# Optimization experiments

Hardware: AMD Instinct MI355X
Metric: run time of the kernel (lower is better)

Reference implementation:

```python
import jax, jax.numpy as jnp
import numpy as np

B, LMAX, T_OUT, VOCAB, EMB, CVEC, HID, OUT = 8192, 12, 10, 36, 300, 256, 256, 512


def setup_inputs() -> dict:
    key = jax.random.key(0)
    ks = jax.random.split(key, 16)
    s = lambda fan: 1.0 / np.sqrt(fan)
    u = lambda k, shape, b: jax.random.uniform(k, shape, jnp.float32, -b, b)
    inp = {
        'words': jax.random.randint(ks[0], (B, LMAX), 0, VOCAB),
        'lengths': 1 + jax.random.randint(ks[1], (B,), 0, LMAX),  # in [1, LMAX]
        'emb_table': jax.random.normal(ks[2], (VOCAB, EMB), jnp.float32),
        'enc_w': u(ks[3], (CVEC, EMB), s(EMB)),
        'enc_b': u(ks[4], (CVEC,), s(EMB)),
        'wih_f': u(ks[5], (4 * HID, CVEC), s(HID)),
        'whh_f': u(ks[6], (4 * HID, HID), s(HID)),
        'bih_f': u(ks[7], (4 * HID,), s(HID)),
        'bhh_f': u(ks[8], (4 * HID,), s(HID)),
        'wih_b': u(ks[9], (4 * HID, CVEC), s(HID)),
        'whh_b': u(ks[10], (4 * HID, HID), s(HID)),
        'bih_b': u(ks[11], (4 * HID,), s(HID)),
        'bhh_b': u(ks[12], (4 * HID,), s(HID)),
        'out_w': u(ks[13], (OUT, 2 * HID), s(2 * HID)),
        'out_b': u(ks[14], (OUT,), s(2 * HID)),
    }
    return inp


def _interp_words(emb_table, words, lengths):
    # bilinear resize (L,300)->(10,300) with align_corners=True; width unchanged
    # so it is exact linear interpolation along the char axis.
    def one(word_row, L):
        Lf = (L - 1).astype(jnp.float32)
        pos = jnp.arange(T_OUT, dtype=jnp.float32) * Lf / (T_OUT - 1)  # (10,)
        i0 = jnp.floor(pos).astype(jnp.int32)
        i1 = jnp.minimum(i0 + 1, L - 1).astype(jnp.int32)
        f = (pos - i0.astype(jnp.float32))[:, None]
        e = emb_table[word_row]  # (LMAX, EMB)
        return e[i0] * (1.0 - f) + e[i1] * f  # (10, EMB)
    return jax.vmap(one)(words, lengths)  # (B, 10, EMB)


def _lstm(seq, wih, whh, bih, bhh):
    # seq: (T, B, In); PyTorch gate order i, f, g, o
    bsz = seq.shape[1]
    h0 = jnp.zeros((bsz, HID), seq.dtype)
    c0 = jnp.zeros((bsz, HID), seq.dtype)

    def step(carry, x_t):
        h, c = carry
        g = x_t @ wih.T + h @ whh.T + (bih + bhh)
        i, f, gg, o = jnp.split(g, 4, axis=-1)
        c = jax.nn.sigmoid(f) * c + jax.nn.sigmoid(i) * jnp.tanh(gg)
        h = jax.nn.sigmoid(o) * jnp.tanh(c)
        return (h, c), h

    _, hs = jax.lax.scan(step, (h0, c0), seq)
    return hs  # (T, B, HID)


def reference(words, lengths, emb_table, enc_w, enc_b, wih_f, whh_f, bih_f, bhh_f,
              wih_b, whh_b, bih_b, bhh_b, out_w, out_b):
    emb = _interp_words(emb_table, words, lengths)              # (B, 10, 300)
    cv = jax.nn.relu(emb @ enc_w.T + enc_b)                     # (B, 10, 256)
    seq = jnp.transpose(cv, (1, 0, 2))                          # (10, B, 256)
    h_f = _lstm(seq, wih_f, whh_f, bih_f, bhh_f)                # (10, B, 256)
    h_b = _lstm(seq[::-1], wih_b, whh_b, bih_b, bhh_b)[::-1]    # (10, B, 256)
    rec = jnp.concatenate([h_f, h_b], axis=-1)                  # (10, B, 512)
    out = rec @ out_w.T + out_b                                 # (10, B, 512)
    return jnp.transpose(out, (1, 0, 2))                        # (B, 10, 512)
```

## Files before the change

### kernel.cpp

```cpp
#include <hip/hip_runtime.h>
#include <hip/hip_fp16.h>

typedef _Float16 f16;
typedef _Float16 f16x2 __attribute__((ext_vector_type(2)));
typedef _Float16 f16x8 __attribute__((ext_vector_type(8)));
typedef float    f32x4 __attribute__((ext_vector_type(4)));

#define NB   8192
#define TOUT 10
#define LMAX 12
#define EMB  300

__device__ __forceinline__ float sigm_(float x) {
    return __builtin_amdgcn_rcpf(1.0f + __builtin_amdgcn_exp2f(x * -1.44269504f));
}
__device__ __forceinline__ float tanh_(float x) {
    return 1.0f - 2.0f * __builtin_amdgcn_rcpf(1.0f + __builtin_amdgcn_exp2f(x * 2.88539008f));
}
__device__ __forceinline__ f16x2 pk_f16(float a, float b) {
    return __builtin_bit_cast(f16x2, __builtin_amdgcn_cvt_pkrtz(a, b));
}

__device__ __forceinline__ void gl_lds16(const f16* g, f16* l) {
    __builtin_amdgcn_global_load_lds(
        (const __attribute__((address_space(1))) void*)g,
        (__attribute__((address_space(3))) void*)l, 16, 0, 0);
}

__global__ __launch_bounds__(256) void pack_w2(
    const float* __restrict__ wih_f, const float* __restrict__ whh_f,
    const float* __restrict__ wih_b, const float* __restrict__ whh_b,
    f16* __restrict__ Wp) {
    int idx = blockIdx.x * 256 + threadIdx.x;
    int d   = idx >> 19;
    int r   = idx & 524287;
    int tile = r >> 9;
    int e    = r & 511;
    int kc = tile >> 6, nt = tile & 63;
    int khi = e >> 7, rem = e & 127, nl = rem >> 3, klo = rem & 7;
    int n = nt * 16 + nl;
    int k = kc * 32 + khi * 8 + klo;
    int gate = (n >> 4) & 3;
    int u = ((n >> 6) << 4) | (n & 15);
    int srow = gate * 256 + u;
    const float* wih = d ? wih_b : wih_f;
    const float* whh = d ? whh_b : whh_f;
    float v = (k < 256) ? wih[srow * 256 + k] : whh[srow * 256 + (k - 256)];
    Wp[idx] = (f16)v;
}

__global__ __launch_bounds__(256) void pack_bias(
    const float* __restrict__ bih_f, const float* __restrict__ bhh_f,
    const float* __restrict__ bih_b, const float* __restrict__ bhh_b,
    float* __restrict__ bp) {
    int idx = blockIdx.x * 256 + threadIdx.x;
    int d = idx >> 10, n = idx & 1023;
    int gate = (n >> 4) & 3;
    int u = ((n >> 6) << 4) | (n & 15);
    int srow = gate * 256 + u;
    bp[idx] = d ? (bih_b[srow] + bhh_b[srow]) : (bih_f[srow] + bhh_f[srow]);
}

__global__ __launch_bounds__(256) void pack_w3(
    const float* __restrict__ out_w, f16* __restrict__ W3p) {
    int idx = blockIdx.x * 256 + threadIdx.x;
    int tile = idx >> 9, e = idx & 511;
    int kc = tile >> 5, nt = tile & 31;
    int khi = e >> 7, rem = e & 127, nl = rem >> 3, klo = rem & 7;
    int n = nt * 16 + nl, k = kc * 32 + khi * 8 + klo;
    W3p[idx] = (f16)out_w[n * 512 + k];
}

__global__ __launch_bounds__(256) void enc_proj(
    const float* __restrict__ tab, const float* __restrict__ ew,
    const float* __restrict__ eb, float* __restrict__ P) {
    int v = blockIdx.x, j = threadIdx.x;
    const float* a = tab + v * EMB;
    const float* w = ew + j * EMB;
    float s = 0.0f;
    for (int k = 0; k < EMB; ++k) s += a[k] * w[k];
    P[v * 256 + j] = s + eb[j];
}

__global__ __launch_bounds__(256) void build_seq(
    const int* __restrict__ words, const int* __restrict__ lengths,
    const float* __restrict__ P, f16* __restrict__ seqp) {
    int gi = blockIdx.x * 256 + threadIdx.x;
    int bl  = gi & 15;
    int khi = (gi >> 4) & 3;
    int kc  = (gi >> 6) & 7;
    int mt  = (gi >> 9) & 511;
    int t   = gi >> 18;
    int b = mt * 16 + bl;
    int L = lengths[b];
    float pos = ((float)t * (float)(L - 1)) / 9.0f;
    int i0 = (int)pos;
    float f = pos - (float)i0;
    int i1 = min(i0 + 1, L - 1);
    int c0 = words[b * LMAX + i0];
    int c1 = words[b * LMAX + i1];
    const float* p0 = P + c0 * 256 + kc * 32 + khi * 8;
    const float* p1 = P + c1 * 256 + kc * 32 + khi * 8;
    f16x8 r;
#pragma unroll
    for (int j = 0; j < 8; ++j) {
        float v = p0[j] * (1.0f - f) + p1[j] * f;
        v = fmaxf(v, 0.0f);
        r[j] = (f16)v;
    }
    *((f16x8*)seqp + gi) = r;
}

__global__ __launch_bounds__(1024) void lstm_fused(
    const f16* __restrict__ seqp, const f16* __restrict__ Wp,
    const float* __restrict__ bp, f16* __restrict__ hcat) {
    const int dir  = blockIdx.x >> 7;
    const int r0t  = (blockIdx.x & 127) << 2;
    const int wave = threadIdx.x >> 6;
    const int lane = threadIdx.x & 63;
    const int l16  = lane & 15;
    const int quad = lane >> 4;

    __shared__ __align__(16) f16 hbuf[2][16384];
    __shared__ __align__(16) f16 sbuf[2][16384];

    {
        f16x8 z = {(f16)0, (f16)0, (f16)0, (f16)0, (f16)0, (f16)0, (f16)0, (f16)0};
        for (int i = threadIdx.x; i < 2048; i += 1024) ((f16x8*)hbuf[0])[i] = z;
    }

    {
        const int t0 = dir ? 9 : 0;
        const f16* s0 = seqp + (size_t)(t0 * 512 + r0t) * 4096;
        gl_lds16(s0 + threadIdx.x * 8,        &sbuf[0][wave * 512]);
        gl_lds16(s0 + 8192 + threadIdx.x * 8, &sbuf[0][8192 + wave * 512]);
    }

    const float* bpd = bp + dir * 1024 + wave * 64;
    float bias_l[4];
#pragma unroll
    for (int nt = 0; nt < 4; ++nt) bias_l[nt] = bpd[nt * 16 + l16];

    const f16* Wu = Wp + dir * 524288 + wave * 2048;
    const int  wo = lane * 8;

    const int slot = wave >> 1;
    const int ofs0 = (((wave & 1) * 2 + (l16 >> 3)) * 16 + quad * 4) * 8 + (l16 & 7);
    const int tile_lo = (r0t * 16 + dir * 8 + slot) * 512;

    float cst[4][4];
#pragma unroll
    for (int m = 0; m < 4; ++m)
#pragma unroll
        for (int q = 0; q < 4; ++q) cst[m][q] = 0.0f;

    __syncthreads();

    int cur = 0;
#pragma unroll 1
    for (int step = 0; step < TOUT; ++step) {
        const int t = dir ? (9 - step) : step;

        if (step != 9) {
            const int tn = dir ? (t - 1) : (t + 1);
            const f16* ns = seqp + (size_t)(tn * 512 + r0t) * 4096;
            gl_lds16(ns + threadIdx.x * 8,        &sbuf[cur ^ 1][wave * 512]);
            gl_lds16(ns + 8192 + threadIdx.x * 8, &sbuf[cur ^ 1][8192 + wave * 512]);
        }

        const f16* sb   = &sbuf[cur][lane * 8];
        const f16* hb_r = &hbuf[cur][lane * 8];
        f16*       hb_w = hbuf[cur ^ 1];

        f32x4 acc[4][4];
#pragma unroll
        for (int m = 0; m < 4; ++m)
#pragma unroll
            for (int nt = 0; nt < 4; ++nt)
#pragma unroll
                for (int q = 0; q < 4; ++q) acc[m][nt][q] = bias_l[nt];

#pragma unroll 1
        for (int kc = 0; kc < 8; ++kc) {
            const f16* wk = Wu + kc * 32768;
            f16x8 bfrag[4];
#pragma unroll
            for (int nt = 0; nt < 4; ++nt)
                bfrag[nt] = *(const f16x8*)(wk + nt * 512 + wo);
            f16x8 afrag[4];
#pragma unroll
            for (int m = 0; m < 4; ++m)
                afrag[m] = *(const f16x8*)(sb + (m * 8 + kc) * 512);
            __builtin_amdgcn_s_setprio(1);
#pragma unroll
            for (int m = 0; m < 4; ++m)
#pragma unroll
                for (int nt = 0; nt < 4; ++nt)
                    acc[m][nt] = __builtin_amdgcn_mfma_f32_16x16x32_f16(
                        afrag[m], bfrag[nt], acc[m][nt], 0, 0, 0);
            __builtin_amdgcn_s_setprio(0);
        }
#pragma unroll 1
        for (int kcl = 0; kcl < 8; ++kcl) {
            const f16* wk = Wu + (kcl + 8) * 32768;
            f16x8 bfrag[4];
#pragma unroll
            for (int nt = 0; nt < 4; ++nt)
                bfrag[nt] = *(const f16x8*)(wk + nt * 512 + wo);
            f16x8 afrag[4];
#pragma unroll
            for (int m = 0; m < 4; ++m)
                afrag[m] = *(const f16x8*)(hb_r + (m * 8 + kcl) * 512);
            __builtin_amdgcn_s_setprio(1);
#pragma unroll
            for (int m = 0; m < 4; ++m)
#pragma unroll
                for (int nt = 0; nt < 4; ++nt)
                    acc[m][nt] = __builtin_amdgcn_mfma_f32_16x16x32_f16(
                        afrag[m], bfrag[nt], acc[m][nt], 0, 0, 0);
            __builtin_amdgcn_s_setprio(0);
        }

        f16* hct = hcat + ((size_t)t * 4194304 + tile_lo);
#pragma unroll
        for (int m = 0; m < 4; ++m) {
#pragma unroll
            for (int q = 0; q < 4; ++q) {
                float iv = acc[m][0][q];
                float fv = acc[m][1][q];
                float gv = acc[m][2][q];
                float ov = acc[m][3][q];
                float c = sigm_(fv) * cst[m][q] + sigm_(iv) * tanh_(gv);
                cst[m][q] = c;
                f16 hv = (f16)(sigm_(ov) * tanh_(c));
                int wt = ofs0 + q * 8;
                hb_w[(m * 8 + slot) * 512 + wt] = hv;
                hct[m * 8192 + wt] = hv;
            }
        }

        __syncthreads();
        cur ^= 1;
    }
}

__global__ __launch_bounds__(512) void out_gemm(
    const f16* __restrict__ hcat, const f16* __restrict__ W3p,
    const float* __restrict__ out_b, float* __restrict__ out) {
    const int mt0  = blockIdx.x << 2;
    const int wave = threadIdx.x >> 6;
    const int lane = threadIdx.x & 63;
    const int l16  = lane & 15;
    const int quad = lane >> 4;
    const int n0   = wave * 64;

    float bias_l[4];
#pragma unroll
    for (int nt = 0; nt < 4; ++nt) bias_l[nt] = out_b[n0 + nt * 16 + l16];

    f32x4 acc[4][4];
#pragma unroll
    for (int m = 0; m < 4; ++m)
#pragma unroll
        for (int nt = 0; nt < 4; ++nt)
#pragma unroll
            for (int q = 0; q < 4; ++q) acc[m][nt][q] = bias_l[nt];

#pragma unroll 2
    for (int kc = 0; kc < 16; ++kc) {
        f16x8 a[4], b[4];
#pragma unroll
        for (int m = 0; m < 4; ++m)
            a[m] = *(const f16x8*)(hcat + ((size_t)((mt0 + m) * 16 + kc) * 512 + lane * 8));
#pragma unroll
        for (int nt = 0; nt < 4; ++nt)
            b[nt] = *(const f16x8*)(W3p + ((kc * 32 + wave * 4 + nt) * 512 + lane * 8));
#pragma unroll
        for (int m = 0; m < 4; ++m)
#pragma unroll
            for (int nt = 0; nt < 4; ++nt)
                acc[m][nt] = __builtin_amdgcn_mfma_f32_16x16x32_f16(a[m], b[nt], acc[m][nt], 0, 0, 0);
    }

#pragma unroll
    for (int m = 0; m < 4; ++m) {
#pragma unroll
        for (int nt = 0; nt < 4; ++nt) {
#pragma unroll
            for (int q = 0; q < 4; ++q) {
                int R = mt0 * 16 + m * 16 + quad * 4 + q;
                int t = R >> 13;
                int b = R & 8191;
                out[(size_t)(b * 10 + t) * 512 + n0 + nt * 16 + l16] = acc[m][nt][q];
            }
        }
    }
}

extern "C" void kernel_launch(void* const* d_in, const int* in_sizes, int n_in,
                              void* d_out, int out_size, void* d_ws, size_t ws_size,
                              hipStream_t stream) {
    const int*   words   = (const int*)d_in[0];
    const int*   lengths = (const int*)d_in[1];
    const float* tab     = (const float*)d_in[2];
    const float* enc_w   = (const float*)d_in[3];
    const float* enc_b   = (const float*)d_in[4];
    const float* wih_f   = (const float*)d_in[5];
    const float* whh_f   = (const float*)d_in[6];
    const float* bih_f   = (const float*)d_in[7];
    const float* bhh_f   = (const float*)d_in[8];
    const float* wih_b   = (const float*)d_in[9];
    const float* whh_b   = (const float*)d_in[10];
    const float* bih_b   = (const float*)d_in[11];
    const float* bhh_b   = (const float*)d_in[12];
    const float* out_w   = (const float*)d_in[13];
    const float* out_b   = (const float*)d_in[14];
    float* out = (float*)d_out;

    char* ws = (char*)d_ws;
    f16*   Wp   = (f16*)(ws + 0);
    f16*   W3p  = (f16*)(ws + 2097152);
    float* bp   = (float*)(ws + 2621440);
    float* P    = (float*)(ws + 2629632);
    f16*   seqp = (f16*)(ws + 2666496);
    f16*   hcat = (f16*)(ws + 44609536);

    pack_w2<<<4096, 256, 0, stream>>>(wih_f, whh_f, wih_b, whh_b, Wp);
    pack_bias<<<8, 256, 0, stream>>>(bih_f, bhh_f, bih_b, bhh_b, bp);
    pack_w3<<<1024, 256, 0, stream>>>(out_w, W3p);
    enc_proj<<<36, 256, 0, stream>>>(tab, enc_w, enc_b, P);
    build_seq<<<10240, 256, 0, stream>>>(words, lengths, P, seqp);
    lstm_fused<<<256, 1024, 0, stream>>>(seqp, Wp, bp, hcat);
    out_gemm<<<1280, 512, 0, stream>>>(hcat, W3p, out_b, out);
}
```

Baseline: 456.4 us.

## Stream LSTM weight fragments through LDS ring with async global-to-LDS loads

Weight B-fragments are no longer loaded straight from global into registers. Each wave now streams them through a small three-slot LDS ring using global_load_lds, with explicit vmcnt waits so the next fragment's load overlaps the current MFMAs. The k-loop is restructured to do the recurrent h part first, then the input sequence part. The sequence tile becomes single-buffered and is loaded at the start of each step instead of prefetched during the previous one. This trades register pressure and global load latency for more LDS traffic and fine-grained waits, and it risks exposing the sequence-load latency and the LDS slot reuse ordering.

```diff
diff --git a/kernel.cpp b/kernel.cpp
--- a/kernel.cpp
+++ b/kernel.cpp
@@ -17,15 +17,14 @@
 __device__ __forceinline__ float tanh_(float x) {
     return 1.0f - 2.0f * __builtin_amdgcn_rcpf(1.0f + __builtin_amdgcn_exp2f(x * 2.88539008f));
 }
-__device__ __forceinline__ f16x2 pk_f16(float a, float b) {
-    return __builtin_bit_cast(f16x2, __builtin_amdgcn_cvt_pkrtz(a, b));
-}
 
 __device__ __forceinline__ void gl_lds16(const f16* g, f16* l) {
     __builtin_amdgcn_global_load_lds(
         (const __attribute__((address_space(1))) void*)g,
         (__attribute__((address_space(3))) void*)l, 16, 0, 0);
 }
+
+#define WAITV(n) asm volatile("s_waitcnt vmcnt(" #n ")" ::: "memory")
 
 __global__ __launch_bounds__(256) void pack_w2(
     const float* __restrict__ wih_f, const float* __restrict__ whh_f,
@@ -122,27 +121,22 @@
     const int quad = lane >> 4;
 
     __shared__ __align__(16) f16 hbuf[2][16384];
-    __shared__ __align__(16) f16 sbuf[2][16384];
+    __shared__ __align__(16) f16 sbuf[16384];
+    __shared__ __align__(16) f16 wbuf[24576];
 
     {
         f16x8 z = {(f16)0, (f16)0, (f16)0, (f16)0, (f16)0, (f16)0, (f16)0, (f16)0};
         for (int i = threadIdx.x; i < 2048; i += 1024) ((f16x8*)hbuf[0])[i] = z;
     }
 
-    {
-        const int t0 = dir ? 9 : 0;
-        const f16* s0 = seqp + (size_t)(t0 * 512 + r0t) * 4096;
-        gl_lds16(s0 + threadIdx.x * 8,        &sbuf[0][wave * 512]);
-        gl_lds16(s0 + 8192 + threadIdx.x * 8, &sbuf[0][8192 + wave * 512]);
-    }
-
     const float* bpd = bp + dir * 1024 + wave * 64;
     float bias_l[4];
 #pragma unroll
     for (int nt = 0; nt < 4; ++nt) bias_l[nt] = bpd[nt * 16 + l16];
 
-    const f16* Wu = Wp + dir * 524288 + wave * 2048;
-    const int  wo = lane * 8;
+    const f16* wsrc = Wp + dir * 524288 + wave * 2048 + lane * 8;
+    f16*       wdst = wbuf + wave * 1536;
+    const f16* wred = wdst + lane * 8;
 
     const int slot = wave >> 1;
     const int ofs0 = (((wave & 1) * 2 + (l16 >> 3)) * 16 + quad * 4) * 8 + (l16 & 7);
@@ -161,17 +155,19 @@
     for (int step = 0; step < TOUT; ++step) {
         const int t = dir ? (9 - step) : step;
 
-        if (step != 9) {
-            const int tn = dir ? (t - 1) : (t + 1);
-            const f16* ns = seqp + (size_t)(tn * 512 + r0t) * 4096;
-            gl_lds16(ns + threadIdx.x * 8,        &sbuf[cur ^ 1][wave * 512]);
-            gl_lds16(ns + 8192 + threadIdx.x * 8, &sbuf[cur ^ 1][8192 + wave * 512]);
-        }
-
-        const f16* sb   = &sbuf[cur][lane * 8];
+        const f16* sb   = &sbuf[lane * 8];
         const f16* hb_r = &hbuf[cur][lane * 8];
         f16*       hb_w = hbuf[cur ^ 1];
 
+        {
+            const f16* ss = seqp + (size_t)(t * 512 + r0t) * 4096;
+            gl_lds16(ss + threadIdx.x * 8,        &sbuf[wave * 512]);
+            gl_lds16(ss + 8192 + threadIdx.x * 8, &sbuf[8192 + wave * 512]);
+        }
+        gl_lds16(wsrc + 8 * 32768 + 0 * 512, wdst + 0 * 512);
+        gl_lds16(wsrc + 8 * 32768 + 1 * 512, wdst + 1 * 512);
+        gl_lds16(wsrc + 8 * 32768 + 2 * 512, wdst + 2 * 512);
+
         f32x4 acc[4][4];
 #pragma unroll
         for (int m = 0; m < 4; ++m)
@@ -180,45 +176,109 @@
 #pragma unroll
                 for (int q = 0; q < 4; ++q) acc[m][nt][q] = bias_l[nt];
 
+        int jm = 0;
 #pragma unroll 1
-        for (int kc = 0; kc < 8; ++kc) {
-            const f16* wk = Wu + kc * 32768;
-            f16x8 bfrag[4];
-#pragma unroll
-            for (int nt = 0; nt < 4; ++nt)
-                bfrag[nt] = *(const f16x8*)(wk + nt * 512 + wo);
+        for (int j = 0; j < 15; ++j) {
+            const f16* ab = (j < 8) ? hb_r : (sb - 4096);
             f16x8 afrag[4];
 #pragma unroll
             for (int m = 0; m < 4; ++m)
-                afrag[m] = *(const f16x8*)(sb + (m * 8 + kc) * 512);
-            __builtin_amdgcn_s_setprio(1);
+                afrag[m] = *(const f16x8*)(ab + (m * 8 + j) * 512);
+
+            int s0 = jm;
+            int s1 = jm + 1; if (s1 >= 3) s1 -= 3;
+            int s2 = jm + 2; if (s2 >= 3) s2 -= 3;
+            const f16* wn0 = wsrc + ((j      ^ 8) * 32768);
+            const f16* wn1 = wsrc + (((j + 1) ^ 8) * 32768);
+
+            WAITV(2);
+            {
+                f16x8 b = *(const f16x8*)(wred + s0 * 512);
+                __builtin_amdgcn_s_setprio(1);
+#pragma unroll
+                for (int m = 0; m < 4; ++m)
+                    acc[m][0] = __builtin_amdgcn_mfma_f32_16x16x32_f16(afrag[m], b, acc[m][0], 0, 0, 0);
+                __builtin_amdgcn_s_setprio(0);
+                gl_lds16(wn0 + 3 * 512, wdst + s0 * 512);
+            }
+            WAITV(2);
+            {
+                f16x8 b = *(const f16x8*)(wred + s1 * 512);
+                __builtin_amdgcn_s_setprio(1);
+#pragma unroll
+                for (int m = 0; m < 4; ++m)
+                    acc[m][1] = __builtin_amdgcn_mfma_f32_16x16x32_f16(afrag[m], b, acc[m][1], 0, 0, 0);
+                __builtin_amdgcn_s_setprio(0);
+                gl_lds16(wn1 + 0 * 512, wdst + s1 * 512);
+            }
+            WAITV(2);
+            {
+                f16x8 b = *(const f16x8*)(wred + s2 * 512);
+                __builtin_amdgcn_s_setprio(1);
+#pragma unroll
+                for (int m = 0; m < 4; ++m)
+                    acc[m][2] = __builtin_amdgcn_mfma_f32_16x16x32_f16(afrag[m], b, acc[m][2], 0, 0, 0);
+                __builtin_amdgcn_s_setprio(0);
+                gl_lds16(wn1 + 1 * 512, wdst + s2 * 512);
+            }
+            WAITV(2);
+            {
+                f16x8 b = *(const f16x8*)(wred + s0 * 512);
+                __builtin_amdgcn_s_setprio(1);
+#pragma unroll
+                for (int m = 0; m < 4; ++m)
+                    acc[m][3] = __builtin_amdgcn_mfma_f32_16x16x32_f16(afrag[m], b, acc[m][3], 0, 0, 0);
+                __builtin_amdgcn_s_setprio(0);
+                gl_lds16(wn1 + 2 * 512, wdst + s0 * 512);
+            }
+            jm = (jm == 2) ? 0 : jm + 1;
+        }
+
+        {
+            const f16* ab = sb - 4096;
+            f16x8 afrag[4];
 #pragma unroll
             for (int m = 0; m < 4; ++m)
-#pragma unroll
-                for (int nt = 0; nt < 4; ++nt)
-                    acc[m][nt] = __builtin_amdgcn_mfma_f32_16x16x32_f16(
-                        afrag[m], bfrag[nt], acc[m][nt], 0, 0, 0);
-            __builtin_amdgcn_s_setprio(0);
-        }
-#pragma unroll 1
-        for (int kcl = 0; kcl < 8; ++kcl) {
-            const f16* wk = Wu + (kcl + 8) * 32768;
-            f16x8 bfrag[4];
-#pragma unroll
-            for (int nt = 0; nt < 4; ++nt)
-                bfrag[nt] = *(const f16x8*)(wk + nt * 512 + wo);
-            f16x8 afrag[4];
-#pragma unroll
-            for (int m = 0; m < 4; ++m)
-                afrag[m] = *(const f16x8*)(hb_r + (m * 8 + kcl) * 512);
-            __builtin_amdgcn_s_setprio(1);
-#pragma unroll
-            for (int m = 0; m < 4; ++m)
-#pragma unroll
-                for (int nt = 0; nt < 4; ++nt)
-                    acc[m][nt] = __builtin_amdgcn_mfma_f32_16x16x32_f16(
-                        afrag[m], bfrag[nt], acc[m][nt], 0, 0, 0);
-            __builtin_amdgcn_s_setprio(0);
+                afrag[m] = *(const f16x8*)(ab + (m * 8 + 15) * 512);
+            const f16* wn0 = wsrc + 7 * 32768;
+
+            WAITV(2);
+            {
+                f16x8 b = *(const f16x8*)(wred + 0 * 512);
+                __builtin_amdgcn_s_setprio(1);
+#pragma unroll
+                for (int m = 0; m < 4; ++m)
+                    acc[m][0] = __builtin_amdgcn_mfma_f32_16x16x32_f16(afrag[m], b, acc[m][0], 0, 0, 0);
+                __builtin_amdgcn_s_setprio(0);
+                gl_lds16(wn0 + 3 * 512, wdst + 0 * 512);
+            }
+            WAITV(2);
+            {
+                f16x8 b = *(const f16x8*)(wred + 1 * 512);
+                __builtin_amdgcn_s_setprio(1);
+#pragma unroll
+                for (int m = 0; m < 4; ++m)
+                    acc[m][1] = __builtin_amdgcn_mfma_f32_16x16x32_f16(afrag[m], b, acc[m][1], 0, 0, 0);
+                __builtin_amdgcn_s_setprio(0);
+            }
+            WAITV(1);
+            {
+                f16x8 b = *(const f16x8*)(wred + 2 * 512);
+                __builtin_amdgcn_s_setprio(1);
+#pragma unroll
+                for (int m = 0; m < 4; ++m)
+                    acc[m][2] = __builtin_amdgcn_mfma_f32_16x16x32_f16(afrag[m], b, acc[m][2], 0, 0, 0);
+                __builtin_amdgcn_s_setprio(0);
+            }
+            WAITV(0);
+            {
+                f16x8 b = *(const f16x8*)(wred + 0 * 512);
+                __builtin_amdgcn_s_setprio(1);
+#pragma unroll
+                for (int m = 0; m < 4; ++m)
+                    acc[m][3] = __builtin_amdgcn_mfma_f32_16x16x32_f16(afrag[m], b, acc[m][3], 0, 0, 0);
+                __builtin_amdgcn_s_setprio(0);
+            }
         }
 
         f16* hct = hcat + ((size_t)t * 4194304 + tile_lo);
```

Measured after the change: 551.3 us. +20.8%, slower.

## Stream LSTM weights through double-buffered LDS and coalesce hidden-state stores

Applied to the files above, without the earlier changes.

The LSTM kernel previously read weight fragments directly from global memory inside each k-chunk loop. It now stages them into a double-buffered LDS area with async global_load_lds, explicitly pipelined over 32 unrolled phases with vmcnt waits. The h and sequence buffers become single-buffered, separated by explicit barriers. The scattered per-element hcat stores are replaced by coalesced 16-byte copies of the previous step's h from LDS. This aims to hide weight-load latency and cut uncoalesced writes, at the cost of more barriers per step and tighter ordering of the vmcnt counts.

```diff
diff --git a/kernel.cpp b/kernel.cpp
--- a/kernel.cpp
+++ b/kernel.cpp
@@ -17,15 +17,14 @@
 __device__ __forceinline__ float tanh_(float x) {
     return 1.0f - 2.0f * __builtin_amdgcn_rcpf(1.0f + __builtin_amdgcn_exp2f(x * 2.88539008f));
 }
-__device__ __forceinline__ f16x2 pk_f16(float a, float b) {
-    return __builtin_bit_cast(f16x2, __builtin_amdgcn_cvt_pkrtz(a, b));
-}
 
 __device__ __forceinline__ void gl_lds16(const f16* g, f16* l) {
     __builtin_amdgcn_global_load_lds(
         (const __attribute__((address_space(1))) void*)g,
         (__attribute__((address_space(3))) void*)l, 16, 0, 0);
 }
+
+#define WAITV(n) asm volatile("s_waitcnt vmcnt(" #n ")" ::: "memory")
 
 __global__ __launch_bounds__(256) void pack_w2(
     const float* __restrict__ wih_f, const float* __restrict__ whh_f,
@@ -121,19 +120,19 @@
     const int l16  = lane & 15;
     const int quad = lane >> 4;
 
-    __shared__ __align__(16) f16 hbuf[2][16384];
-    __shared__ __align__(16) f16 sbuf[2][16384];
+    __shared__ __align__(16) f16 hbuf[16384];
+    __shared__ __align__(16) f16 sbuf[16384];
+    __shared__ __align__(16) f16 wbuf[2][16384];
 
     {
         f16x8 z = {(f16)0, (f16)0, (f16)0, (f16)0, (f16)0, (f16)0, (f16)0, (f16)0};
-        for (int i = threadIdx.x; i < 2048; i += 1024) ((f16x8*)hbuf[0])[i] = z;
-    }
-
+        for (int i = threadIdx.x; i < 2048; i += 1024) ((f16x8*)hbuf)[i] = z;
+    }
     {
         const int t0 = dir ? 9 : 0;
         const f16* s0 = seqp + (size_t)(t0 * 512 + r0t) * 4096;
-        gl_lds16(s0 + threadIdx.x * 8,        &sbuf[0][wave * 512]);
-        gl_lds16(s0 + 8192 + threadIdx.x * 8, &sbuf[0][8192 + wave * 512]);
+        gl_lds16(s0 + threadIdx.x * 8,        &sbuf[wave * 512]);
+        gl_lds16(s0 + 8192 + threadIdx.x * 8, &sbuf[8192 + wave * 512]);
     }
 
     const float* bpd = bp + dir * 1024 + wave * 64;
@@ -141,12 +140,15 @@
 #pragma unroll
     for (int nt = 0; nt < 4; ++nt) bias_l[nt] = bpd[nt * 16 + l16];
 
-    const f16* Wu = Wp + dir * 524288 + wave * 2048;
-    const int  wo = lane * 8;
+    const f16* Wsl = Wp + dir * 524288 + wave * 2048 + lane * 8;
+    f16*       wds = &wbuf[0][wave * 1024];
+    const f16* wbr = &wbuf[0][wave * 1024 + lane * 8];
+
+    const f16* sbl = sbuf + lane * 8;
+    const f16* hbl = hbuf + lane * 8;
 
     const int slot = wave >> 1;
     const int ofs0 = (((wave & 1) * 2 + (l16 >> 3)) * 16 + quad * 4) * 8 + (l16 & 7);
-    const int tile_lo = (r0t * 16 + dir * 8 + slot) * 512;
 
     float cst[4][4];
 #pragma unroll
@@ -154,74 +156,94 @@
 #pragma unroll
         for (int q = 0; q < 4; ++q) cst[m][q] = 0.0f;
 
+    gl_lds16(Wsl + 0 * 512, wds);
+    gl_lds16(Wsl + 1 * 512, wds + 512);
+    gl_lds16(Wsl + 2 * 512, wds + 16384);
+    gl_lds16(Wsl + 3 * 512, wds + 16384 + 512);
+
     __syncthreads();
 
-    int cur = 0;
+#define PHASE(P)  do {                                                         \
+    if ((P) == 31) { WAITV(0); } else { WAITV(2); }                            \
+    const f16* br_ = wbr + ((P) & 1) * 16384;                                  \
+    f16x8 b0_ = *(const f16x8*)(br_);                                          \
+    f16x8 b1_ = *(const f16x8*)(br_ + 512);                                    \
+    if (((P) & 1) == 0) {                                                      \
+        const f16* ab_ = (((P) >> 1) < 8) ? sbl : hbl;                         \
+        const int ko_ = ((P) >> 1) & 7;                                        \
+        af0 = *(const f16x8*)(ab_ + (0 * 8 + ko_) * 512);                      \
+        af1 = *(const f16x8*)(ab_ + (1 * 8 + ko_) * 512);                      \
+        af2 = *(const f16x8*)(ab_ + (2 * 8 + ko_) * 512);                      \
+        af3 = *(const f16x8*)(ab_ + (3 * 8 + ko_) * 512);                      \
+    }                                                                          \
+    __builtin_amdgcn_s_setprio(1);                                             \
+    acc[0][((P)&1)*2]   = __builtin_amdgcn_mfma_f32_16x16x32_f16(af0, b0_, acc[0][((P)&1)*2],   0,0,0); \
+    acc[1][((P)&1)*2]   = __builtin_amdgcn_mfma_f32_16x16x32_f16(af1, b0_, acc[1][((P)&1)*2],   0,0,0); \
+    acc[2][((P)&1)*2]   = __builtin_amdgcn_mfma_f32_16x16x32_f16(af2, b0_, acc[2][((P)&1)*2],   0,0,0); \
+    acc[3][((P)&1)*2]   = __builtin_amdgcn_mfma_f32_16x16x32_f16(af3, b0_, acc[3][((P)&1)*2],   0,0,0); \
+    acc[0][((P)&1)*2+1] = __builtin_amdgcn_mfma_f32_16x16x32_f16(af0, b1_, acc[0][((P)&1)*2+1], 0,0,0); \
+    acc[1][((P)&1)*2+1] = __builtin_amdgcn_mfma_f32_16x16x32_f16(af1, b1_, acc[1][((P)&1)*2+1], 0,0,0); \
+    acc[2][((P)&1)*2+1] = __builtin_amdgcn_mfma_f32_16x16x32_f16(af2, b1_, acc[2][((P)&1)*2+1], 0,0,0); \
+    acc[3][((P)&1)*2+1] = __builtin_amdgcn_mfma_f32_16x16x32_f16(af3, b1_, acc[3][((P)&1)*2+1], 0,0,0); \
+    __builtin_amdgcn_s_setprio(0);                                             \
+    if ((P) < 30) {                                                            \
+        f16* wd_ = wds + ((P) & 1) * 16384;                                    \
+        gl_lds16(Wsl + ((((P) + 2) >> 1) * 64 + (((P) + 2) & 1) * 2) * 512,       wd_);       \
+        gl_lds16(Wsl + ((((P) + 2) >> 1) * 64 + (((P) + 2) & 1) * 2 + 1) * 512,   wd_ + 512); \
+    }                                                                          \
+} while (0)
+
+    int step = 0;
 #pragma unroll 1
-    for (int step = 0; step < TOUT; ++step) {
+    for (; step < TOUT; ++step) {
         const int t = dir ? (9 - step) : step;
 
+        f32x4 acc[4][4];
+#pragma unroll
+        for (int m = 0; m < 4; ++m)
+#pragma unroll
+            for (int nt = 0; nt < 4; ++nt)
+#pragma unroll
+                for (int q = 0; q < 4; ++q) acc[m][nt][q] = bias_l[nt];
+
+        f16x8 af0, af1, af2, af3;
+
+        PHASE(0);  PHASE(1);  PHASE(2);  PHASE(3);
+        PHASE(4);  PHASE(5);  PHASE(6);  PHASE(7);
+        PHASE(8);  PHASE(9);  PHASE(10); PHASE(11);
+        PHASE(12); PHASE(13); PHASE(14); PHASE(15);
+
+        __builtin_amdgcn_s_barrier();
         if (step != 9) {
             const int tn = dir ? (t - 1) : (t + 1);
             const f16* ns = seqp + (size_t)(tn * 512 + r0t) * 4096;
-            gl_lds16(ns + threadIdx.x * 8,        &sbuf[cur ^ 1][wave * 512]);
-            gl_lds16(ns + 8192 + threadIdx.x * 8, &sbuf[cur ^ 1][8192 + wave * 512]);
-        }
-
-        const f16* sb   = &sbuf[cur][lane * 8];
-        const f16* hb_r = &hbuf[cur][lane * 8];
-        f16*       hb_w = hbuf[cur ^ 1];
-
-        f32x4 acc[4][4];
-#pragma unroll
-        for (int m = 0; m < 4; ++m)
-#pragma unroll
-            for (int nt = 0; nt < 4; ++nt)
-#pragma unroll
-                for (int q = 0; q < 4; ++q) acc[m][nt][q] = bias_l[nt];
-
-#pragma unroll 1
-        for (int kc = 0; kc < 8; ++kc) {
-            const f16* wk = Wu + kc * 32768;
-            f16x8 bfrag[4];
-#pragma unroll
-            for (int nt = 0; nt < 4; ++nt)
-                bfrag[nt] = *(const f16x8*)(wk + nt * 512 + wo);
-            f16x8 afrag[4];
-#pragma unroll
-            for (int m = 0; m < 4; ++m)
-                afrag[m] = *(const f16x8*)(sb + (m * 8 + kc) * 512);
-            __builtin_amdgcn_s_setprio(1);
-#pragma unroll
-            for (int m = 0; m < 4; ++m)
-#pragma unroll
-                for (int nt = 0; nt < 4; ++nt)
-                    acc[m][nt] = __builtin_amdgcn_mfma_f32_16x16x32_f16(
-                        afrag[m], bfrag[nt], acc[m][nt], 0, 0, 0);
-            __builtin_amdgcn_s_setprio(0);
-        }
-#pragma unroll 1
-        for (int kcl = 0; kcl < 8; ++kcl) {
-            const f16* wk = Wu + (kcl + 8) * 32768;
-            f16x8 bfrag[4];
-#pragma unroll
-            for (int nt = 0; nt < 4; ++nt)
-                bfrag[nt] = *(const f16x8*)(wk + nt * 512 + wo);
-            f16x8 afrag[4];
-#pragma unroll
-            for (int m = 0; m < 4; ++m)
-                afrag[m] = *(const f16x8*)(hb_r + (m * 8 + kcl) * 512);
-            __builtin_amdgcn_s_setprio(1);
-#pragma unroll
-            for (int m = 0; m < 4; ++m)
-#pragma unroll
-                for (int nt = 0; nt < 4; ++nt)
-                    acc[m][nt] = __builtin_amdgcn_mfma_f32_16x16x32_f16(
-                        afrag[m], bfrag[nt], acc[m][nt], 0, 0, 0);
-            __builtin_amdgcn_s_setprio(0);
-        }
-
-        f16* hct = hcat + ((size_t)t * 4194304 + tile_lo);
+            gl_lds16(ns + threadIdx.x * 8,        &sbuf[wave * 512]);
+            gl_lds16(ns + 8192 + threadIdx.x * 8, &sbuf[8192 + wave * 512]);
+        }
+
+        PHASE(16); PHASE(17); PHASE(18); PHASE(19);
+        PHASE(20); PHASE(21); PHASE(22); PHASE(23);
+        PHASE(24); PHASE(25); PHASE(26); PHASE(27);
+        PHASE(28); PHASE(29); PHASE(30); PHASE(31);
+
+        if (step != 0) {
+            const int tp = dir ? (t + 1) : (t - 1);
+#pragma unroll
+            for (int e0 = 0; e0 < 2; ++e0) {
+                const int e = (int)threadIdx.x + e0 * 1024;
+                f16x8 v = ((const f16x8*)hbuf)[e];
+                ((f16x8*)hcat)[((size_t)(tp * 512 + r0t + (e >> 9)) * 16 + dir * 8) * 64 + (e & 511)] = v;
+            }
+        }
+        if (step != 9) {
+            gl_lds16(Wsl + 0 * 512, wds);
+            gl_lds16(Wsl + 1 * 512, wds + 512);
+            gl_lds16(Wsl + 2 * 512, wds + 16384);
+            gl_lds16(Wsl + 3 * 512, wds + 16384 + 512);
+        }
+
+        __builtin_amdgcn_s_barrier();
+
 #pragma unroll
         for (int m = 0; m < 4; ++m) {
 #pragma unroll
@@ -232,15 +254,22 @@
                 float ov = acc[m][3][q];
                 float c = sigm_(fv) * cst[m][q] + sigm_(iv) * tanh_(gv);
                 cst[m][q] = c;
-                f16 hv = (f16)(sigm_(ov) * tanh_(c));
-                int wt = ofs0 + q * 8;
-                hb_w[(m * 8 + slot) * 512 + wt] = hv;
-                hct[m * 8192 + wt] = hv;
+                hbuf[(m * 8 + slot) * 512 + ofs0 + q * 8] = (f16)(sigm_(ov) * tanh_(c));
             }
         }
 
         __syncthreads();
-        cur ^= 1;
+    }
+#undef PHASE
+
+    {
+        const int tl = dir ? 0 : 9;
+#pragma unroll
+        for (int e0 = 0; e0 < 2; ++e0) {
+            const int e = (int)threadIdx.x + e0 * 1024;
+            f16x8 v = ((const f16x8*)hbuf)[e];
+            ((f16x8*)hcat)[((size_t)(tl * 512 + r0t + (e >> 9)) * 16 + dir * 8) * 64 + (e & 511)] = v;
+        }
     }
 }
 
```

Result: slower. 725.7 us (+59.0%).

## Split LSTM gate GEMM into two half passes with register-prefetched weights

Applied to the files above, without the earlier changes.

Gate rows are reordered so that (i,g) and (f,o) sit in adjacent column tiles. Each step then runs two half-width MFMA passes: the first computes sigmoid(i)*tanh(g) into a small buffer, and the second finishes the cell update. This halves the live accumulator registers at 1024 threads per block. The weight fragments are software-pipelined, with the next k-chunk loaded during the current MFMAs. The prefetch of the next timestep's input into LDS is moved later in the step. The cost is reloading the A fragments from LDS twice per step and a more intricate schedule.

```diff
diff --git a/kernel.cpp b/kernel.cpp
--- a/kernel.cpp
+++ b/kernel.cpp
@@ -16,9 +16,6 @@
 }
 __device__ __forceinline__ float tanh_(float x) {
     return 1.0f - 2.0f * __builtin_amdgcn_rcpf(1.0f + __builtin_amdgcn_exp2f(x * 2.88539008f));
-}
-__device__ __forceinline__ f16x2 pk_f16(float a, float b) {
-    return __builtin_bit_cast(f16x2, __builtin_amdgcn_cvt_pkrtz(a, b));
 }
 
 __device__ __forceinline__ void gl_lds16(const f16* g, f16* l) {
@@ -40,9 +37,10 @@
     int khi = e >> 7, rem = e & 127, nl = rem >> 3, klo = rem & 7;
     int n = nt * 16 + nl;
     int k = kc * 32 + khi * 8 + klo;
-    int gate = (n >> 4) & 3;
+    int gp = (n >> 4) & 3;
+    int sg = ((gp & 1) << 1) | (gp >> 1);
     int u = ((n >> 6) << 4) | (n & 15);
-    int srow = gate * 256 + u;
+    int srow = sg * 256 + u;
     const float* wih = d ? wih_b : wih_f;
     const float* whh = d ? whh_b : whh_f;
     float v = (k < 256) ? wih[srow * 256 + k] : whh[srow * 256 + (k - 256)];
@@ -55,9 +53,10 @@
     float* __restrict__ bp) {
     int idx = blockIdx.x * 256 + threadIdx.x;
     int d = idx >> 10, n = idx & 1023;
-    int gate = (n >> 4) & 3;
+    int gp = (n >> 4) & 3;
+    int sg = ((gp & 1) << 1) | (gp >> 1);
     int u = ((n >> 6) << 4) | (n & 15);
-    int srow = gate * 256 + u;
+    int srow = sg * 256 + u;
     bp[idx] = d ? (bih_b[srow] + bhh_b[srow]) : (bih_f[srow] + bhh_f[srow]);
 }
 
@@ -128,7 +127,6 @@
         f16x8 z = {(f16)0, (f16)0, (f16)0, (f16)0, (f16)0, (f16)0, (f16)0, (f16)0};
         for (int i = threadIdx.x; i < 2048; i += 1024) ((f16x8*)hbuf[0])[i] = z;
     }
-
     {
         const int t0 = dir ? 9 : 0;
         const f16* s0 = seqp + (size_t)(t0 * 512 + r0t) * 4096;
@@ -141,8 +139,7 @@
 #pragma unroll
     for (int nt = 0; nt < 4; ++nt) bias_l[nt] = bpd[nt * 16 + l16];
 
-    const f16* Wu = Wp + dir * 524288 + wave * 2048;
-    const int  wo = lane * 8;
+    const f16* Wsl = Wp + dir * 524288 + wave * 2048 + lane * 8;
 
     const int slot = wave >> 1;
     const int ofs0 = (((wave & 1) * 2 + (l16 >> 3)) * 16 + quad * 4) * 8 + (l16 & 7);
@@ -155,93 +152,115 @@
         for (int q = 0; q < 4; ++q) cst[m][q] = 0.0f;
 
     __syncthreads();
+
+#define KLOOP(PB, acc)                                                         \
+    {                                                                          \
+        f16x8 bE0 = *(const f16x8*)(Wsl + (PB) * 512);                         \
+        f16x8 bE1 = *(const f16x8*)(Wsl + ((PB) + 1) * 512);                   \
+        f16x8 bO0 = *(const f16x8*)(Wsl + 32768 + (PB) * 512);                 \
+        f16x8 bO1 = *(const f16x8*)(Wsl + 32768 + ((PB) + 1) * 512);           \
+        _Pragma("unroll 1")                                                    \
+        for (int k2 = 0; k2 < 8; ++k2) {                                       \
+            const f16* ab = (k2 < 4) ? sbl : hbl;                              \
+            const int ke = (2 * k2) & 7, ko = (2 * k2 + 1) & 7;                \
+            f16x8 a0 = *(const f16x8*)(ab + (0 * 8 + ke) * 512);               \
+            f16x8 a1 = *(const f16x8*)(ab + (1 * 8 + ke) * 512);               \
+            f16x8 a2 = *(const f16x8*)(ab + (2 * 8 + ke) * 512);               \
+            f16x8 a3 = *(const f16x8*)(ab + (3 * 8 + ke) * 512);               \
+            __builtin_amdgcn_s_setprio(1);                                     \
+            acc[0][0] = __builtin_amdgcn_mfma_f32_16x16x32_f16(a0, bE0, acc[0][0], 0, 0, 0); \
+            acc[1][0] = __builtin_amdgcn_mfma_f32_16x16x32_f16(a1, bE0, acc[1][0], 0, 0, 0); \
+            acc[2][0] = __builtin_amdgcn_mfma_f32_16x16x32_f16(a2, bE0, acc[2][0], 0, 0, 0); \
+            acc[3][0] = __builtin_amdgcn_mfma_f32_16x16x32_f16(a3, bE0, acc[3][0], 0, 0, 0); \
+            acc[0][1] = __builtin_amdgcn_mfma_f32_16x16x32_f16(a0, bE1, acc[0][1], 0, 0, 0); \
+            acc[1][1] = __builtin_amdgcn_mfma_f32_16x16x32_f16(a1, bE1, acc[1][1], 0, 0, 0); \
+            acc[2][1] = __builtin_amdgcn_mfma_f32_16x16x32_f16(a2, bE1, acc[2][1], 0, 0, 0); \
+            acc[3][1] = __builtin_amdgcn_mfma_f32_16x16x32_f16(a3, bE1, acc[3][1], 0, 0, 0); \
+            __builtin_amdgcn_s_setprio(0);                                     \
+            if (k2 < 7) {       \
+                const f16* wn = Wsl + (2 * k2 + 2) * 32768;                    \
+                bE0 = *(const f16x8*)(wn + (PB) * 512);                        \
+                bE1 = *(const f16x8*)(wn + ((PB) + 1) * 512);                  \
+            }                                                                  \
+            a0 = *(const f16x8*)(ab + (0 * 8 + ko) * 512);                     \
+            a1 = *(const f16x8*)(ab + (1 * 8 + ko) * 512);                     \
+            a2 = *(const f16x8*)(ab + (2 * 8 + ko) * 512);                     \
+            a3 = *(const f16x8*)(ab + (3 * 8 + ko) * 512);                     \
+            __builtin_amdgcn_s_setprio(1);                                     \
+            acc[0][0] = __builtin_amdgcn_mfma_f32_16x16x32_f16(a0, bO0, acc[0][0], 0, 0, 0); \
+            acc[1][0] = __builtin_amdgcn_mfma_f32_16x16x32_f16(a1, bO0, acc[1][0], 0, 0, 0); \
+            acc[2][0] = __builtin_amdgcn_mfma_f32_16x16x32_f16(a2, bO0, acc[2][0], 0, 0, 0); \
+            acc[3][0] = __builtin_amdgcn_mfma_f32_16x16x32_f16(a3, bO0, acc[3][0], 0, 0, 0); \
+            acc[0][1] = __builtin_amdgcn_mfma_f32_16x16x32_f16(a0, bO1, acc[0][1], 0, 0, 0); \
+            acc[1][1] = __builtin_amdgcn_mfma_f32_16x16x32_f16(a1, bO1, acc[1][1], 0, 0, 0); \
+            acc[2][1] = __builtin_amdgcn_mfma_f32_16x16x32_f16(a2, bO1, acc[2][1], 0, 0, 0); \
+            acc[3][1] = __builtin_amdgcn_mfma_f32_16x16x32_f16(a3, bO1, acc[3][1], 0, 0, 0); \
+            __builtin_amdgcn_s_setprio(0);                                     \
+            if (k2 < 7) {        \
+                const f16* wn = Wsl + (2 * k2 + 3) * 32768;                    \
+                bO0 = *(const f16x8*)(wn + (PB) * 512);                        \
+                bO1 = *(const f16x8*)(wn + ((PB) + 1) * 512);                  \
+            }                                                                  \
+        }                                                                      \
+    }
 
     int cur = 0;
 #pragma unroll 1
     for (int step = 0; step < TOUT; ++step) {
         const int t = dir ? (9 - step) : step;
-
-        if (step != 9) {
-            const int tn = dir ? (t - 1) : (t + 1);
-            const f16* ns = seqp + (size_t)(tn * 512 + r0t) * 4096;
-            gl_lds16(ns + threadIdx.x * 8,        &sbuf[cur ^ 1][wave * 512]);
-            gl_lds16(ns + 8192 + threadIdx.x * 8, &sbuf[cur ^ 1][8192 + wave * 512]);
+        const f16* sbl = sbuf[cur] + lane * 8;
+        const f16* hbl = hbuf[cur] + lane * 8;
+        f16*       hb_w = hbuf[cur ^ 1];
+
+        float z[4][4];
+        {
+            f32x4 acc[4][2];
+#pragma unroll
+            for (int m = 0; m < 4; ++m)
+#pragma unroll
+                for (int q = 0; q < 4; ++q) { acc[m][0][q] = bias_l[0]; acc[m][1][q] = bias_l[1]; }
+            KLOOP(0, acc);
+#pragma unroll
+            for (int m = 0; m < 4; ++m)
+#pragma unroll
+                for (int q = 0; q < 4; ++q)
+                    z[m][q] = sigm_(acc[m][0][q]) * tanh_(acc[m][1][q]);
         }
 
-        const f16* sb   = &sbuf[cur][lane * 8];
-        const f16* hb_r = &hbuf[cur][lane * 8];
-        f16*       hb_w = hbuf[cur ^ 1];
-
-        f32x4 acc[4][4];
-#pragma unroll
-        for (int m = 0; m < 4; ++m)
-#pragma unroll
-            for (int nt = 0; nt < 4; ++nt)
-#pragma unroll
-                for (int q = 0; q < 4; ++q) acc[m][nt][q] = bias_l[nt];
-
-#pragma unroll 1
-        for (int kc = 0; kc < 8; ++kc) {
-            const f16* wk = Wu + kc * 32768;
-            f16x8 bfrag[4];
-#pragma unroll
-            for (int nt = 0; nt < 4; ++nt)
-                bfrag[nt] = *(const f16x8*)(wk + nt * 512 + wo);
-            f16x8 afrag[4];
+        {
+            f32x4 acc[4][2];
 #pragma unroll
             for (int m = 0; m < 4; ++m)
-                afrag[m] = *(const f16x8*)(sb + (m * 8 + kc) * 512);
-            __builtin_amdgcn_s_setprio(1);
-#pragma unroll
-            for (int m = 0; m < 4; ++m)
-#pragma unroll
-                for (int nt = 0; nt < 4; ++nt)
-                    acc[m][nt] = __builtin_amdgcn_mfma_f32_16x16x32_f16(
-                        afrag[m], bfrag[nt], acc[m][nt], 0, 0, 0);
-            __builtin_amdgcn_s_setprio(0);
-        }
-#pragma unroll 1
-        for (int kcl = 0; kcl < 8; ++kcl) {
-            const f16* wk = Wu + (kcl + 8) * 32768;
-            f16x8 bfrag[4];
-#pragma unroll
-            for (int nt = 0; nt < 4; ++nt)
-                bfrag[nt] = *(const f16x8*)(wk + nt * 512 + wo);
-            f16x8 afrag[4];
-#pragma unroll
-            for (int m = 0; m < 4; ++m)
-                afrag[m] = *(const f16x8*)(hb_r + (m * 8 + kcl) * 512);
-            __builtin_amdgcn_s_setprio(1);
-#pragma unroll
-            for (int m = 0; m < 4; ++m)
-#pragma unroll
-                for (int nt = 0; nt < 4; ++nt)
-                    acc[m][nt] = __builtin_amdgcn_mfma_f32_16x16x32_f16(
-                        afrag[m], bfrag[nt], acc[m][nt], 0, 0, 0);
-            __builtin_amdgcn_s_setprio(0);
-        }
-
-        f16* hct = hcat + ((size_t)t * 4194304 + tile_lo);
-#pragma unroll
-        for (int m = 0; m < 4; ++m) {
-#pragma unroll
-            for (int q = 0; q < 4; ++q) {
-                float iv = acc[m][0][q];
-                float fv = acc[m][1][q];
-                float gv = acc[m][2][q];
-                float ov = acc[m][3][q];
-                float c = sigm_(fv) * cst[m][q] + sigm_(iv) * tanh_(gv);
-                cst[m][q] = c;
-                f16 hv = (f16)(sigm_(ov) * tanh_(c));
-                int wt = ofs0 + q * 8;
-                hb_w[(m * 8 + slot) * 512 + wt] = hv;
-                hct[m * 8192 + wt] = hv;
+#pragma unroll
+                for (int q = 0; q < 4; ++q) { acc[m][0][q] = bias_l[2]; acc[m][1][q] = bias_l[3]; }
+            KLOOP(2, acc);
+
+            if (step != 9) {
+                const int tn = dir ? (t - 1) : (t + 1);
+                const f16* ns = seqp + (size_t)(tn * 512 + r0t) * 4096;
+                gl_lds16(ns + threadIdx.x * 8,        &sbuf[cur ^ 1][wave * 512]);
+                gl_lds16(ns + 8192 + threadIdx.x * 8, &sbuf[cur ^ 1][8192 + wave * 512]);
+            }
+
+            f16* hct = hcat + ((size_t)t * 4194304 + tile_lo);
+#pragma unroll
+            for (int m = 0; m < 4; ++m) {
+#pragma unroll
+                for (int q = 0; q < 4; ++q) {
+                    float c = sigm_(acc[m][0][q]) * cst[m][q] + z[m][q];
+                    cst[m][q] = c;
+                    f16 hv = (f16)(sigm_(acc[m][1][q]) * tanh_(c));
+                    int wt = ofs0 + q * 8;
+                    hb_w[(m * 8 + slot) * 512 + wt] = hv;
+                    hct[m * 8192 + wt] = hv;
+                }
             }
         }
 
         __syncthreads();
         cur ^= 1;
     }
+#undef KLOOP
 }
 
 __global__ __launch_bounds__(512) void out_gemm(
```

New measurement: 511.2 us. +12.0%, slower.
